# Optimization experiments

Measured on AMD Instinct MI355X. Metric: run time of the kernel, lower is better.

The kernel has to match this reference:

```python
import jax, jax.numpy as jnp
import numpy as np

B, T, C = 4, 2048, 1024
H = 16
HD = C // H  # 64


def setup_inputs() -> dict:
    key = jax.random.key(0)
    k1, k2, k3, k4, k5 = jax.random.split(key, 5)
    x = jax.random.normal(k1, (B, T, C), dtype=jnp.float32)
    W_qkv = jax.random.normal(k2, (3 * C, C), dtype=jnp.float32) * (1.0 / np.sqrt(C))
    W_proj = jax.random.normal(k3, (C, C), dtype=jnp.float32) * (1.0 / np.sqrt(C))
    # realistic RoPE tables
    pos = jnp.arange(T, dtype=jnp.float32)[:, None]
    inv_freq = 1.0 / (10000.0 ** (jnp.arange(0, HD, 2, dtype=jnp.float32) / HD))
    ang = pos * inv_freq[None, :]  # [T, HD//2]
    cos = jnp.cos(ang)
    sin = jnp.sin(ang)
    mask = jnp.ones((1, 1, T, T), dtype=jnp.int32)
    return {"x": x, "W_qkv": W_qkv, "W_proj": W_proj, "cos": cos, "sin": sin, "mask": mask}


def _apply_rope(xh, cos, sin):
    # xh: [B, H, T, HD]; cos/sin: [T, HD//2]
    b, h, t, hd = xh.shape
    xr = xh.reshape(b, h, t, hd // 2, 2)
    x1, x2 = xr[..., 0], xr[..., 1]
    c = cos[:t][None, None, :, :]
    s = sin[:t][None, None, :, :]
    o1 = x1 * c - x2 * s
    o2 = x1 * s + x2 * c
    return jnp.stack([o1, o2], axis=-1).reshape(b, h, t, hd)


def reference(x, W_qkv, W_proj, cos, sin, mask):
    b, t, c = x.shape
    qkv = jnp.einsum('btc,dc->btd', x, W_qkv)  # Linear: x @ W^T
    qkv = qkv.reshape(b, t, 3, H, HD).transpose(2, 0, 3, 1, 4)  # [3, B, H, T, HD]
    q, k, v = qkv[0], qkv[1], qkv[2]
    q = _apply_rope(q, cos, sin)
    k = _apply_rope(k, cos, sin)
    scale = 1.0 / np.sqrt(HD)
    attn = jnp.einsum('bhqd,bhkd->bhqk', q, k) * scale
    attn = jnp.where(mask == 0, -jnp.inf, attn)
    attn = jax.nn.softmax(attn, axis=-1)
    out = jnp.einsum('bhqk,bhkd->bhqd', attn, v)
    out = out.transpose(0, 2, 1, 3).reshape(b, t, c)
    out = jnp.einsum('btc,dc->btd', out, W_proj)
    return out
```

## Files before the change

### kernel.cpp

```cpp
#include <hip/hip_runtime.h>
#include <hip/hip_bf16.h>
#include <cstdint>
#include <cstddef>

typedef __attribute__((ext_vector_type(8))) short s16x8;
typedef __attribute__((ext_vector_type(4))) float f32x4;
typedef __attribute__((ext_vector_type(16))) float f32x16;
typedef __attribute__((ext_vector_type(4))) unsigned u32x4;
typedef __attribute__((ext_vector_type(4))) unsigned short us16x4;

#define DEVI static __device__ __forceinline__

DEVI short f2bf(float f) {
  unsigned u = __builtin_bit_cast(unsigned, f);
  u += 0x7fffu + ((u >> 16) & 1u);
  return (short)(u >> 16);
}
DEVI unsigned pack2(float a, float b) {
  return (unsigned)(unsigned short)f2bf(a) | ((unsigned)(unsigned short)f2bf(b) << 16);
}
DEVI f32x4 mfma16(s16x8 a, s16x8 b, f32x4 c) {
  return __builtin_amdgcn_mfma_f32_16x16x32_bf16(a, b, c, 0, 0, 0);
}
DEVI f32x16 mfma32(s16x8 a, s16x8 b, f32x16 c) {
  return __builtin_amdgcn_mfma_f32_32x32x16_bf16(a, b, c, 0, 0, 0);
}
DEVI void gload16(const short* src, short* dst) {
  __builtin_amdgcn_global_load_lds(
      (const __attribute__((address_space(1))) unsigned*)src,
      (__attribute__((address_space(3))) unsigned*)dst, 16, 0, 0);
}
DEVI float expfast(float x) {
  float r; asm("v_exp_f32 %0, %1" : "=v"(r) : "v"(x)); return r;
}
DEVI unsigned cvtpk(float lo, float hi) {
  unsigned r; asm("v_cvt_pk_bf16_f32 %0, %1, %2" : "=v"(r) : "v"(lo), "v"(hi)); return r;
}
DEVI float max3f(float a, float b, float c) {
  float r; asm("v_max3_f32 %0, %1, %2, %3" : "=v"(r) : "v"(a), "v"(b), "v"(c)); return r;
}

__global__ __launch_bounds__(256) void cvt_kernel(
    const float* __restrict__ x, const float* __restrict__ wq,
    const float* __restrict__ wp, short* __restrict__ xb,
    short* __restrict__ wqb, short* __restrict__ wpb)
{
  const long long stride = (long long)gridDim.x * blockDim.x;
  for (long long i = (long long)blockIdx.x * blockDim.x + threadIdx.x;
       i < 1572864; i += stride) {
    const float* src; short* dst; long long off;
    if (i < 1048576)      { src = x;  dst = xb;  off = i; }
    else if (i < 1441792) { src = wq; dst = wqb; off = i - 1048576; }
    else                  { src = wp; dst = wpb; off = i - 1441792; }
    const float4 a = *reinterpret_cast<const float4*>(src + off * 8);
    const float4 b = *reinterpret_cast<const float4*>(src + off * 8 + 4);
    u32x4 o = {pack2(a.x, a.y), pack2(a.z, a.w), pack2(b.x, b.y), pack2(b.z, b.w)};
    *reinterpret_cast<u32x4*>(dst + off * 8) = o;
  }
}

__global__ __launch_bounds__(256, 4) void qkv_rope_b16_kernel(
    const short* __restrict__ xb, const short* __restrict__ wqb,
    const float* __restrict__ cosT, const float* __restrict__ sinT,
    short* __restrict__ qw, short* __restrict__ kw, short* __restrict__ vw)
{
  __shared__ short As[128 * 32];
  __shared__ short Bs[128 * 32];
  const int tid = threadIdx.x;
  const int lane = tid & 63, w = tid >> 6;
  const int wr = w >> 1, wc = w & 1;
  const int l15 = lane & 15, l4 = lane >> 4;
  const int m0 = blockIdx.x * 128;
  const int n0 = blockIdx.y * 128;
  const int lrow = lane >> 2, lslot = (lane & 3) * 8;

  f32x4 acc[4][4];
#pragma unroll
  for (int i = 0; i < 4; i++)
#pragma unroll
    for (int j = 0; j < 4; j++) acc[i][j] = (f32x4){0.f, 0.f, 0.f, 0.f};

  for (int k0 = 0; k0 < 1024; k0 += 32) {
    if (k0) __syncthreads();
#pragma unroll
    for (int half = 0; half < 2; half++) {
      const int rbase = half * 64 + w * 16;
      gload16(xb + (size_t)(m0 + rbase + lrow) * 1024 + k0 + lslot, As + rbase * 32);
      gload16(wqb + (size_t)(n0 + rbase + lrow) * 1024 + k0 + lslot, Bs + rbase * 32);
    }
    __syncthreads();
    s16x8 af[4], bf[4];
#pragma unroll
    for (int i = 0; i < 4; i++)
      af[i] = *reinterpret_cast<const s16x8*>(As + (wr * 64 + i * 16 + l15) * 32 + l4 * 8);
#pragma unroll
    for (int j = 0; j < 4; j++)
      bf[j] = *reinterpret_cast<const s16x8*>(Bs + (wc * 64 + j * 16 + l15) * 32 + l4 * 8);
#pragma unroll
    for (int i = 0; i < 4; i++)
#pragma unroll
      for (int j = 0; j < 4; j++)
        acc[i][j] = mfma16(af[i], bf[j], acc[i][j]);
  }

#pragma unroll
  for (int j = 0; j < 4; j++) {
    const int gn = n0 + wc * 64 + j * 16 + l15;
    const int three = gn >> 10;
    const int h = (gn >> 6) & 15;
    const int hd = gn & 63;
    short* dst = three == 0 ? qw : (three == 1 ? kw : vw);
    const bool isqk = three < 2;
    const int ii = hd >> 1;
    const int odd = hd & 1;
#pragma unroll
    for (int i = 0; i < 4; i++) {
#pragma unroll
      for (int r = 0; r < 4; r++) {
        const int gm = m0 + wr * 64 + i * 16 + l4 * 4 + r;
        const int b = gm >> 11;
        const int t = gm & 2047;
        float v = acc[i][j][r];
        float other = __shfl_xor(v, 1, 64);
        if (isqk) {
          float c = cosT[t * 32 + ii];
          float s = sinT[t * 32 + ii];
          v = odd ? (other * s + v * c) : (v * c - other * s);
        }
        if (three == 0) v *= 0.18033688f;
        dst[((size_t)((b * 16 + h) * 2048 + t) << 6) + hd] = f2bf(v);
      }
    }
  }
}

__global__ __launch_bounds__(256, 4) void proj_b16_kernel(
    const short* __restrict__ ao, const short* __restrict__ wpb,
    float* __restrict__ out)
{
  __shared__ short As[128 * 32];
  __shared__ short Bs[128 * 32];
  const int tid = threadIdx.x;
  const int lane = tid & 63, w = tid >> 6;
  const int wr = w >> 1, wc = w & 1;
  const int l15 = lane & 15, l4 = lane >> 4;
  const int m0 = blockIdx.x * 128;
  const int n0 = blockIdx.y * 128;
  const int lrow = lane >> 2, lslot = (lane & 3) * 8;

  f32x4 acc[4][4];
#pragma unroll
  for (int i = 0; i < 4; i++)
#pragma unroll
    for (int j = 0; j < 4; j++) acc[i][j] = (f32x4){0.f, 0.f, 0.f, 0.f};

  for (int k0 = 0; k0 < 1024; k0 += 32) {
    if (k0) __syncthreads();
#pragma unroll
    for (int half = 0; half < 2; half++) {
      const int rbase = half * 64 + w * 16;
      gload16(ao + (size_t)(m0 + rbase + lrow) * 1024 + k0 + lslot, As + rbase * 32);
      gload16(wpb + (size_t)(n0 + rbase + lrow) * 1024 + k0 + lslot, Bs + rbase * 32);
    }
    __syncthreads();
    s16x8 af[4], bf[4];
#pragma unroll
    for (int i = 0; i < 4; i++)
      af[i] = *reinterpret_cast<const s16x8*>(As + (wr * 64 + i * 16 + l15) * 32 + l4 * 8);
#pragma unroll
    for (int j = 0; j < 4; j++)
      bf[j] = *reinterpret_cast<const s16x8*>(Bs + (wc * 64 + j * 16 + l15) * 32 + l4 * 8);
#pragma unroll
    for (int i = 0; i < 4; i++)
#pragma unroll
      for (int j = 0; j < 4; j++)
        acc[i][j] = mfma16(af[i], bf[j], acc[i][j]);
  }

#pragma unroll
  for (int i = 0; i < 4; i++)
#pragma unroll
    for (int j = 0; j < 4; j++)
#pragma unroll
      for (int r = 0; r < 4; r++) {
        int gm = m0 + wr * 64 + i * 16 + l4 * 4 + r;
        int gn = n0 + wc * 64 + j * 16 + l15;
        out[(size_t)gm * 1024 + gn] = acc[i][j][r];
      }
}

__global__ __launch_bounds__(256, 2) void qkv_rope_kernel(
    const float* __restrict__ x, const float* __restrict__ W,
    const float* __restrict__ cosT, const float* __restrict__ sinT,
    short* __restrict__ qw, short* __restrict__ kw, short* __restrict__ vw)
{
  __shared__ short As[128][40];
  __shared__ short Bs[128][40];
  const int tid = threadIdx.x;
  const int lane = tid & 63, w = tid >> 6;
  const int wr = w >> 1, wc = w & 1;
  const int l15 = lane & 15, l4 = lane >> 4;
  const int m0 = blockIdx.x * 128;
  const int n0 = blockIdx.y * 128;

  f32x4 acc[4][4];
#pragma unroll
  for (int i = 0; i < 4; i++)
#pragma unroll
    for (int j = 0; j < 4; j++) acc[i][j] = (f32x4){0.f, 0.f, 0.f, 0.f};

  for (int k0 = 0; k0 < 1024; k0 += 32) {
    if (k0) __syncthreads();
#pragma unroll
    for (int i = 0; i < 4; i++) {
      int c = tid + 256 * i;
      int row = c >> 3, co = (c & 7) * 4;
      const float4 va = *reinterpret_cast<const float4*>(x + (size_t)(m0 + row) * 1024 + k0 + co);
      const float4 vb = *reinterpret_cast<const float4*>(W + (size_t)(n0 + row) * 1024 + k0 + co);
      uint2 pa; pa.x = pack2(va.x, va.y); pa.y = pack2(va.z, va.w);
      uint2 pb; pb.x = pack2(vb.x, vb.y); pb.y = pack2(vb.z, vb.w);
      *reinterpret_cast<uint2*>(&As[row][co]) = pa;
      *reinterpret_cast<uint2*>(&Bs[row][co]) = pb;
    }
    __syncthreads();
    s16x8 af[4], bf[4];
#pragma unroll
    for (int i = 0; i < 4; i++)
      af[i] = *reinterpret_cast<const s16x8*>(&As[wr * 64 + i * 16 + l15][l4 * 8]);
#pragma unroll
    for (int j = 0; j < 4; j++)
      bf[j] = *reinterpret_cast<const s16x8*>(&Bs[wc * 64 + j * 16 + l15][l4 * 8]);
#pragma unroll
    for (int i = 0; i < 4; i++)
#pragma unroll
      for (int j = 0; j < 4; j++)
        acc[i][j] = mfma16(af[i], bf[j], acc[i][j]);
  }

#pragma unroll
  for (int j = 0; j < 4; j++) {
    const int gn = n0 + wc * 64 + j * 16 + l15;
    const int three = gn >> 10;
    const int h = (gn >> 6) & 15;
    const int hd = gn & 63;
    short* dst = three == 0 ? qw : (three == 1 ? kw : vw);
    const bool isqk = three < 2;
    const int ii = hd >> 1;
    const int odd = hd & 1;
#pragma unroll
    for (int i = 0; i < 4; i++) {
#pragma unroll
      for (int r = 0; r < 4; r++) {
        const int gm = m0 + wr * 64 + i * 16 + l4 * 4 + r;
        const int b = gm >> 11;
        const int t = gm & 2047;
        float v = acc[i][j][r];
        float other = __shfl_xor(v, 1, 64);
        if (isqk) {
          float c = cosT[t * 32 + ii];
          float s = sinT[t * 32 + ii];
          v = odd ? (other * s + v * c) : (v * c - other * s);
        }
        if (three == 0) v *= 0.18033688f;
        dst[((size_t)((b * 16 + h) * 2048 + t) << 6) + hd] = f2bf(v);
      }
    }
  }
}

__global__ __launch_bounds__(256, 2) void proj_kernel(
    const short* __restrict__ ao, const float* __restrict__ W, float* __restrict__ out)
{
  __shared__ short As[128][40];
  __shared__ short Bs[128][40];
  const int tid = threadIdx.x;
  const int lane = tid & 63, w = tid >> 6;
  const int wr = w >> 1, wc = w & 1;
  const int l15 = lane & 15, l4 = lane >> 4;
  const int m0 = blockIdx.x * 128;
  const int n0 = blockIdx.y * 128;

  f32x4 acc[4][4];
#pragma unroll
  for (int i = 0; i < 4; i++)
#pragma unroll
    for (int j = 0; j < 4; j++) acc[i][j] = (f32x4){0.f, 0.f, 0.f, 0.f};

  for (int k0 = 0; k0 < 1024; k0 += 32) {
    if (k0) __syncthreads();
#pragma unroll
    for (int i = 0; i < 2; i++) {
      int c = tid + 256 * i;
      int row = c >> 2, co = (c & 3) * 8;
      *reinterpret_cast<s16x8*>(&As[row][co]) =
          *reinterpret_cast<const s16x8*>(ao + (size_t)(m0 + row) * 1024 + k0 + co);
    }
#pragma unroll
    for (int i = 0; i < 4; i++) {
      int c = tid + 256 * i;
      int row = c >> 3, co = (c & 7) * 4;
      const float4 vb = *reinterpret_cast<const float4*>(W + (size_t)(n0 + row) * 1024 + k0 + co);
      uint2 pb; pb.x = pack2(vb.x, vb.y); pb.y = pack2(vb.z, vb.w);
      *reinterpret_cast<uint2*>(&Bs[row][co]) = pb;
    }
    __syncthreads();
    s16x8 af[4], bf[4];
#pragma unroll
    for (int i = 0; i < 4; i++)
      af[i] = *reinterpret_cast<const s16x8*>(&As[wr * 64 + i * 16 + l15][l4 * 8]);
#pragma unroll
    for (int j = 0; j < 4; j++)
      bf[j] = *reinterpret_cast<const s16x8*>(&Bs[wc * 64 + j * 16 + l15][l4 * 8]);
#pragma unroll
    for (int i = 0; i < 4; i++)
#pragma unroll
      for (int j = 0; j < 4; j++)
        acc[i][j] = mfma16(af[i], bf[j], acc[i][j]);
  }

#pragma unroll
  for (int i = 0; i < 4; i++)
#pragma unroll
    for (int j = 0; j < 4; j++)
#pragma unroll
      for (int r = 0; r < 4; r++) {
        int gm = m0 + wr * 64 + i * 16 + l4 * 4 + r;
        int gn = n0 + wc * 64 + j * 16 + l15;
        out[(size_t)gm * 1024 + gn] = acc[i][j][r];
      }
}

__global__ __launch_bounds__(512, 4) void attn_kernel(
    const short* __restrict__ qw, const short* __restrict__ kw,
    const short* __restrict__ vw, short* __restrict__ ao)
{
  __shared__ short lds[24576];
  unsigned* lds32 = (unsigned*)lds;

  const int tid = threadIdx.x;
  const int lane = tid & 63, w = tid >> 6;
  const int l31 = lane & 31, hi = lane >> 5;

  const int fid = blockIdx.y * 8 + blockIdx.x;
  const int qx = (fid >> 3) & 7;
  const int bh = (fid & 7) | ((fid >> 6) << 3);
  const int q0 = qx * 256;
  const size_t base = (size_t)bh << 17;

  const int qrow = q0 + w * 32 + l31;
  s16x8 qf[4];
#pragma unroll
  for (int ds = 0; ds < 4; ds++)
    qf[ds] = *reinterpret_cast<const s16x8*>(qw + base + (size_t)qrow * 64 + ds * 16 + hi * 8);

  const int krow = w * 8 + (lane >> 3);
  const int kslot = lane & 7;
  const int vp = tid & 31;
  const int vd4 = (tid >> 5) * 4;

  auto stageK = [&](int buf, int kv0) {
    short* dst = &lds[buf * 4096 + w * 512];
    const short* src = kw + base + (size_t)(kv0 + krow) * 64 + ((kslot ^ (krow & 7)) * 8);
    gload16(src, dst);
  };
  auto loadV = [&](int kv0, us16x4& lo, us16x4& hi4) {
    const short* s0 = vw + base + (size_t)(kv0 + 2 * vp) * 64 + vd4;
    lo  = *reinterpret_cast<const us16x4*>(s0);
    hi4 = *reinterpret_cast<const us16x4*>(s0 + 64);
  };
  auto writeV = [&](int buf, us16x4 lo, us16x4 hi4) {
#pragma unroll
    for (int i = 0; i < 4; i++) {
      int d = vd4 + i;
      unsigned val = (unsigned)lo[i] | ((unsigned)hi4[i] << 16);
      lds32[4096 + buf * 2048 + d * 32 + (vp ^ ((d & 7) << 2))] = val;
    }
  };

  unsigned* Pw = lds32 + 8192 + w * 512 + l31 * 16;
  const int qsw = (l31 >> 1) & 3;

  f32x16 o0, o1;
#pragma unroll
  for (int r = 0; r < 16; r++) { o0[r] = 0.f; o1[r] = 0.f; }
  float m_run = -1e30f, l_run = 0.f;

  {
    us16x4 lo, hh;
    loadV(0, lo, hh);
    stageK(0, 0);
    writeV(0, lo, hh);
  }
  __syncthreads();

  const int NT = 32;
  for (int kt = 0; kt < NT; kt++) {
    const int cur = kt & 1;
    us16x4 vlo, vhi;
    const bool more = (kt + 1) < NT;
    if (more) {
      loadV((kt + 1) * 64, vlo, vhi);
      stageK(cur ^ 1, (kt + 1) * 64);
    }

    const short* Kbuf = &lds[cur * 4096];
    f32x16 S0, S1;
#pragma unroll
    for (int r = 0; r < 16; r++) { S0[r] = 0.f; S1[r] = 0.f; }
    __builtin_amdgcn_s_setprio(1);
#pragma unroll
    for (int ds = 0; ds < 4; ds++) {
      const int slot = ((ds * 2 + hi) ^ (l31 & 7)) * 8;
      s16x8 a0 = *reinterpret_cast<const s16x8*>(Kbuf + l31 * 64 + slot);
      s16x8 a1 = *reinterpret_cast<const s16x8*>(Kbuf + (32 + l31) * 64 + slot);
      S0 = mfma32(a0, qf[ds], S0);
      S1 = mfma32(a1, qf[ds], S1);
    }
    __builtin_amdgcn_s_setprio(0);

    float a0m = max3f(S0[0], S0[1], S0[2]);
    float a1m = max3f(S0[3], S0[4], S0[5]);
    float a2m = max3f(S0[6], S0[7], S0[8]);
    float a3m = max3f(S0[9], S0[10], S0[11]);
    float a4m = max3f(S0[12], S0[13], S0[14]);
    float a5m = max3f(S0[15], S1[0], S1[1]);
    float a6m = max3f(S1[2], S1[3], S1[4]);
    float a7m = max3f(S1[5], S1[6], S1[7]);
    float a8m = max3f(S1[8], S1[9], S1[10]);
    float a9m = max3f(S1[11], S1[12], S1[13]);
    float aam = fmaxf(S1[14], S1[15]);
    float b0m = max3f(a0m, a1m, a2m);
    float b1m = max3f(a3m, a4m, a5m);
    float b2m = max3f(a6m, a7m, a8m);
    float b3m = fmaxf(a9m, aam);
    float mx = fmaxf(max3f(b0m, b1m, b2m), b3m);
    mx = fmaxf(mx, __shfl_xor(mx, 32, 64));

    if (!__all(mx - m_run <= 8.0f)) {
      const float mnew = fmaxf(m_run, mx);
      const float corr = expfast(m_run - mnew);
      m_run = mnew;
      l_run *= corr;
#pragma unroll
      for (int r = 0; r < 16; r++) { o0[r] *= corr; o1[r] *= corr; }
    }
    float s0a = 0.f, s1a = 0.f, s2a = 0.f, s3a = 0.f;
#pragma unroll
    for (int r = 0; r < 16; r += 4) {
      S0[r+0] = expfast(S0[r+0] - m_run); s0a += S0[r+0];
      S0[r+1] = expfast(S0[r+1] - m_run); s1a += S0[r+1];
      S0[r+2] = expfast(S0[r+2] - m_run); s2a += S0[r+2];
      S0[r+3] = expfast(S0[r+3] - m_run); s3a += S0[r+3];
    }
#pragma unroll
    for (int r = 0; r < 16; r += 4) {
      S1[r+0] = expfast(S1[r+0] - m_run); s0a += S1[r+0];
      S1[r+1] = expfast(S1[r+1] - m_run); s1a += S1[r+1];
      S1[r+2] = expfast(S1[r+2] - m_run); s2a += S1[r+2];
      S1[r+3] = expfast(S1[r+3] - m_run); s3a += S1[r+3];
    }
    float sum = (s0a + s1a) + (s2a + s3a);
    sum += __shfl_xor(sum, 32, 64);
    l_run += sum;

    if (more) writeV(cur ^ 1, vlo, vhi);

    const short* Vbuf = &lds[8192 + cur * 4096];
    auto doHalf = [&](const f32x16& Sh, int sbase) {
      __builtin_amdgcn_s_setprio(1);
#pragma unroll
      for (int g2 = 0; g2 < 4; g2++) {
        uint2 val;
        val.x = cvtpk(Sh[4 * g2 + 0], Sh[4 * g2 + 1]);
        val.y = cvtpk(Sh[4 * g2 + 2], Sh[4 * g2 + 3]);
        *reinterpret_cast<uint2*>(Pw + ((g2 ^ qsw) << 2) + 2 * hi) = val;
      }
#pragma unroll
      for (int sp = 0; sp < 2; sp++) {
        const int s = sbase + sp;
        u32x4 praw = *reinterpret_cast<const u32x4*>(Pw + (((2 * sp + hi) ^ qsw) << 2));
        s16x8 bfrag = __builtin_bit_cast(s16x8, praw);
        const int kvslot = ((s * 2 + hi) ^ (l31 & 7)) * 8;
        s16x8 v0 = *reinterpret_cast<const s16x8*>(Vbuf + l31 * 64 + kvslot);
        s16x8 v1 = *reinterpret_cast<const s16x8*>(Vbuf + (32 + l31) * 64 + kvslot);
        o0 = mfma32(v0, bfrag, o0);
        o1 = mfma32(v1, bfrag, o1);
      }
      __builtin_amdgcn_s_setprio(0);
    };
    doHalf(S0, 0);
    doHalf(S1, 2);

    __syncthreads();
  }

  const float rl = 1.0f / l_run;
  {
    const int q = l31;
#pragma unroll
    for (int dt = 0; dt < 2; dt++) {
#pragma unroll
      for (int rg = 0; rg < 4; rg++) {
        const int d = dt * 32 + 8 * rg + 4 * hi;
        float a0 = (dt ? o1[rg*4+0] : o0[rg*4+0]) * rl;
        float a1 = (dt ? o1[rg*4+1] : o0[rg*4+1]) * rl;
        float a2 = (dt ? o1[rg*4+2] : o0[rg*4+2]) * rl;
        float a3 = (dt ? o1[rg*4+3] : o0[rg*4+3]) * rl;
        const int sidx0 = w * 2048 + q * 64 + (d ^ ((q & 7) << 3));
        const int sidx1 = w * 2048 + q * 64 + ((d + 2) ^ ((q & 7) << 3));
        lds32[sidx0 >> 1] = pack2(a0, a1);
        lds32[sidx1 >> 1] = pack2(a2, a3);
      }
    }
  }
  __syncthreads();
  const int b = bh >> 4, h = bh & 15;
#pragma unroll
  for (int i = 0; i < 4; i++) {
    const int idx = i * 4096 + tid * 8;
    const int wi = idx >> 11;
    const int rem = idx & 2047;
    const int q = rem >> 6;
    const int d8 = rem & 63;
    s16x8 vv = *reinterpret_cast<const s16x8*>(&lds[wi * 2048 + q * 64 + (d8 ^ ((q & 7) << 3))]);
    const int row = q0 + wi * 32 + q;
    *reinterpret_cast<s16x8*>(ao + (size_t)(b * 2048 + row) * 1024 + h * 64 + d8) = vv;
  }
}

extern "C" void kernel_launch(void* const* d_in, const int* in_sizes, int n_in,
                              void* d_out, int out_size, void* d_ws, size_t ws_size,
                              hipStream_t stream) {
  const float* x     = (const float*)d_in[0];
  const float* Wqkv  = (const float*)d_in[1];
  const float* Wproj = (const float*)d_in[2];
  const float* cosT  = (const float*)d_in[3];
  const float* sinT  = (const float*)d_in[4];
  float* out = (float*)d_out;

  const size_t NEL = (size_t)4 * 16 * 2048 * 64;
  short* qw = (short*)d_ws;
  short* kw = qw + NEL;
  short* vw = kw + NEL;
  short* ao = vw + NEL;
  short* xb  = ao + NEL;
  short* wqb = xb + 8388608;
  short* wpb = wqb + 3145728;
  const size_t need = (4 * NEL + 8388608 + 3145728 + 1048576) * sizeof(short);

  if (ws_size >= need) {
    cvt_kernel<<<2048, 256, 0, stream>>>(x, Wqkv, Wproj, xb, wqb, wpb);
    qkv_rope_b16_kernel<<<dim3(64, 24), 256, 0, stream>>>(xb, wqb, cosT, sinT, qw, kw, vw);
    attn_kernel<<<dim3(8, 64), 512, 0, stream>>>(qw, kw, vw, ao);
    proj_b16_kernel<<<dim3(64, 8), 256, 0, stream>>>(ao, wpb, out);
  } else {
    qkv_rope_kernel<<<dim3(64, 24), 256, 0, stream>>>(x, Wqkv, cosT, sinT, qw, kw, vw);
    attn_kernel<<<dim3(8, 64), 512, 0, stream>>>(qw, kw, vw, ao);
    proj_kernel<<<dim3(64, 8), 256, 0, stream>>>(ao, Wproj, out);
  }
}
```

Before: 202.7 us.

## Double-buffer LDS, swizzle tiles, and remap blocks to XCDs in bf16 GEMMs

Both bf16 GEMM kernels (QKV+RoPE and output projection) now double-buffer their LDS tiles, so the next K-slice loads while MFMAs run on the current one, leaving one barrier per iteration instead of two. The LDS layout gets an XOR swizzle on the 8-element column slot to cut bank conflicts on fragment reads. The grid is flattened to 1D and remapped so blocks landing on the same XCD share N-tiles of the weight matrix, for better L2 reuse. LDS per block doubles to 32KB, which may limit occupancy at 4 blocks per CU.

```diff
diff --git a/kernel.cpp b/kernel.cpp
--- a/kernel.cpp
+++ b/kernel.cpp
@@ -64,48 +64,63 @@
     const float* __restrict__ cosT, const float* __restrict__ sinT,
     short* __restrict__ qw, short* __restrict__ kw, short* __restrict__ vw)
 {
-  __shared__ short As[128 * 32];
-  __shared__ short Bs[128 * 32];
+  __shared__ short As[2][128 * 32];
+  __shared__ short Bs[2][128 * 32];
   const int tid = threadIdx.x;
   const int lane = tid & 63, w = tid >> 6;
   const int wr = w >> 1, wc = w & 1;
   const int l15 = lane & 15, l4 = lane >> 4;
-  const int m0 = blockIdx.x * 128;
-  const int n0 = blockIdx.y * 128;
-  const int lrow = lane >> 2, lslot = (lane & 3) * 8;
+
+  const int bid = blockIdx.x;
+  const int xcd = bid & 7, j = bid >> 3;
+  const int n0 = (xcd * 3 + (j >> 6)) * 128;
+  const int m0 = (j & 63) * 128;
+
+  const int gr = lane >> 2;
+  const int sl = lane & 3;
+  const int skey = (lane >> 3) & 3;
+  const int scol = (sl ^ skey) * 8;
+  const int rsw = (l15 >> 1) & 3;
+
+  auto stage = [&](int buf, int k0) {
+#pragma unroll
+    for (int g = 0; g < 2; g++) {
+      const int rbase = w * 32 + g * 16;
+      gload16(xb + (size_t)(m0 + rbase + gr) * 1024 + k0 + scol, &As[buf][rbase * 32]);
+      gload16(wqb + (size_t)(n0 + rbase + gr) * 1024 + k0 + scol, &Bs[buf][rbase * 32]);
+    }
+  };
 
   f32x4 acc[4][4];
 #pragma unroll
   for (int i = 0; i < 4; i++)
 #pragma unroll
-    for (int j = 0; j < 4; j++) acc[i][j] = (f32x4){0.f, 0.f, 0.f, 0.f};
-
-  for (int k0 = 0; k0 < 1024; k0 += 32) {
-    if (k0) __syncthreads();
-#pragma unroll
-    for (int half = 0; half < 2; half++) {
-      const int rbase = half * 64 + w * 16;
-      gload16(xb + (size_t)(m0 + rbase + lrow) * 1024 + k0 + lslot, As + rbase * 32);
-      gload16(wqb + (size_t)(n0 + rbase + lrow) * 1024 + k0 + lslot, Bs + rbase * 32);
-    }
+    for (int j2 = 0; j2 < 4; j2++) acc[i][j2] = (f32x4){0.f, 0.f, 0.f, 0.f};
+
+  stage(0, 0);
+  __syncthreads();
+
+  for (int t = 0; t < 32; t++) {
+    const int cur = t & 1;
+    if (t + 1 < 32) stage(cur ^ 1, (t + 1) * 32);
+    s16x8 af[4], bf[4];
+#pragma unroll
+    for (int i = 0; i < 4; i++)
+      af[i] = *reinterpret_cast<const s16x8*>(&As[cur][(wr * 64 + i * 16 + l15) * 32 + ((l4 ^ rsw) * 8)]);
+#pragma unroll
+    for (int j2 = 0; j2 < 4; j2++)
+      bf[j2] = *reinterpret_cast<const s16x8*>(&Bs[cur][(wc * 64 + j2 * 16 + l15) * 32 + ((l4 ^ rsw) * 8)]);
+#pragma unroll
+    for (int i = 0; i < 4; i++)
+#pragma unroll
+      for (int j2 = 0; j2 < 4; j2++)
+        acc[i][j2] = mfma16(af[i], bf[j2], acc[i][j2]);
     __syncthreads();
-    s16x8 af[4], bf[4];
-#pragma unroll
-    for (int i = 0; i < 4; i++)
-      af[i] = *reinterpret_cast<const s16x8*>(As + (wr * 64 + i * 16 + l15) * 32 + l4 * 8);
-#pragma unroll
-    for (int j = 0; j < 4; j++)
-      bf[j] = *reinterpret_cast<const s16x8*>(Bs + (wc * 64 + j * 16 + l15) * 32 + l4 * 8);
-#pragma unroll
-    for (int i = 0; i < 4; i++)
-#pragma unroll
-      for (int j = 0; j < 4; j++)
-        acc[i][j] = mfma16(af[i], bf[j], acc[i][j]);
-  }
-
-#pragma unroll
-  for (int j = 0; j < 4; j++) {
-    const int gn = n0 + wc * 64 + j * 16 + l15;
+  }
+
+#pragma unroll
+  for (int j2 = 0; j2 < 4; j2++) {
+    const int gn = n0 + wc * 64 + j2 * 16 + l15;
     const int three = gn >> 10;
     const int h = (gn >> 6) & 15;
     const int hd = gn & 63;
@@ -119,16 +134,16 @@
       for (int r = 0; r < 4; r++) {
         const int gm = m0 + wr * 64 + i * 16 + l4 * 4 + r;
         const int b = gm >> 11;
-        const int t = gm & 2047;
-        float v = acc[i][j][r];
+        const int t2 = gm & 2047;
+        float v = acc[i][j2][r];
         float other = __shfl_xor(v, 1, 64);
         if (isqk) {
-          float c = cosT[t * 32 + ii];
-          float s = sinT[t * 32 + ii];
+          float c = cosT[t2 * 32 + ii];
+          float s = sinT[t2 * 32 + ii];
           v = odd ? (other * s + v * c) : (v * c - other * s);
         }
         if (three == 0) v *= 0.18033688f;
-        dst[((size_t)((b * 16 + h) * 2048 + t) << 6) + hd] = f2bf(v);
+        dst[((size_t)((b * 16 + h) * 2048 + t2) << 6) + hd] = f2bf(v);
       }
     }
   }
@@ -138,15 +153,29 @@
     const short* __restrict__ ao, const short* __restrict__ wpb,
     float* __restrict__ out)
 {
-  __shared__ short As[128 * 32];
-  __shared__ short Bs[128 * 32];
+  __shared__ short As[2][128 * 32];
+  __shared__ short Bs[2][128 * 32];
   const int tid = threadIdx.x;
   const int lane = tid & 63, w = tid >> 6;
   const int wr = w >> 1, wc = w & 1;
   const int l15 = lane & 15, l4 = lane >> 4;
-  const int m0 = blockIdx.x * 128;
-  const int n0 = blockIdx.y * 128;
-  const int lrow = lane >> 2, lslot = (lane & 3) * 8;
+
+  const int bid = blockIdx.x;
+  const int n0 = (bid & 7) * 128;
+  const int m0 = (bid >> 3) * 128;
+
+  const int gr = lane >> 2;
+  const int scol = ((lane & 3) ^ ((lane >> 3) & 3)) * 8;
+  const int rsw = (l15 >> 1) & 3;
+
+  auto stage = [&](int buf, int k0) {
+#pragma unroll
+    for (int g = 0; g < 2; g++) {
+      const int rbase = w * 32 + g * 16;
+      gload16(ao + (size_t)(m0 + rbase + gr) * 1024 + k0 + scol, &As[buf][rbase * 32]);
+      gload16(wpb + (size_t)(n0 + rbase + gr) * 1024 + k0 + scol, &Bs[buf][rbase * 32]);
+    }
+  };
 
   f32x4 acc[4][4];
 #pragma unroll
@@ -154,27 +183,25 @@
 #pragma unroll
     for (int j = 0; j < 4; j++) acc[i][j] = (f32x4){0.f, 0.f, 0.f, 0.f};
 
-  for (int k0 = 0; k0 < 1024; k0 += 32) {
-    if (k0) __syncthreads();
-#pragma unroll
-    for (int half = 0; half < 2; half++) {
-      const int rbase = half * 64 + w * 16;
-      gload16(ao + (size_t)(m0 + rbase + lrow) * 1024 + k0 + lslot, As + rbase * 32);
-      gload16(wpb + (size_t)(n0 + rbase + lrow) * 1024 + k0 + lslot, Bs + rbase * 32);
-    }
-    __syncthreads();
+  stage(0, 0);
+  __syncthreads();
+
+  for (int t = 0; t < 32; t++) {
+    const int cur = t & 1;
+    if (t + 1 < 32) stage(cur ^ 1, (t + 1) * 32);
     s16x8 af[4], bf[4];
 #pragma unroll
     for (int i = 0; i < 4; i++)
-      af[i] = *reinterpret_cast<const s16x8*>(As + (wr * 64 + i * 16 + l15) * 32 + l4 * 8);
+      af[i] = *reinterpret_cast<const s16x8*>(&As[cur][(wr * 64 + i * 16 + l15) * 32 + ((l4 ^ rsw) * 8)]);
 #pragma unroll
     for (int j = 0; j < 4; j++)
-      bf[j] = *reinterpret_cast<const s16x8*>(Bs + (wc * 64 + j * 16 + l15) * 32 + l4 * 8);
+      bf[j] = *reinterpret_cast<const s16x8*>(&Bs[cur][(wc * 64 + j * 16 + l15) * 32 + ((l4 ^ rsw) * 8)]);
 #pragma unroll
     for (int i = 0; i < 4; i++)
 #pragma unroll
       for (int j = 0; j < 4; j++)
         acc[i][j] = mfma16(af[i], bf[j], acc[i][j]);
+    __syncthreads();
   }
 
 #pragma unroll
@@ -550,9 +577,9 @@
 
   if (ws_size >= need) {
     cvt_kernel<<<2048, 256, 0, stream>>>(x, Wqkv, Wproj, xb, wqb, wpb);
-    qkv_rope_b16_kernel<<<dim3(64, 24), 256, 0, stream>>>(xb, wqb, cosT, sinT, qw, kw, vw);
+    qkv_rope_b16_kernel<<<1536, 256, 0, stream>>>(xb, wqb, cosT, sinT, qw, kw, vw);
     attn_kernel<<<dim3(8, 64), 512, 0, stream>>>(qw, kw, vw, ao);
-    proj_b16_kernel<<<dim3(64, 8), 256, 0, stream>>>(ao, wpb, out);
+    proj_b16_kernel<<<512, 256, 0, stream>>>(ao, wpb, out);
   } else {
     qkv_rope_kernel<<<dim3(64, 24), 256, 0, stream>>>(x, Wqkv, cosT, sinT, qw, kw, vw);
     attn_kernel<<<dim3(8, 64), 512, 0, stream>>>(qw, kw, vw, ao);
```

New measurement: 226.7 us. 1.12x slower.
